# Kernel tuning notes

Measured on AMD Instinct MI355X. Metric: run time of the kernel, lower is better.

## Reference

```python
import jax, jax.numpy as jnp
import numpy as np
from jax import lax

L, H, DH, D, FF = 8, 16, 64, 1024, 4096  # layers, heads, head dim, model dim, mlp hidden
B, S = 4, 512
EPS = 1e-5


def setup_inputs() -> dict:
    key = jax.random.key(0)
    ks = jax.random.split(key, 8)
    std = 0.02
    return {
        "x": jax.random.normal(ks[0], (B, S, D), jnp.float32),
        "ln1_w": jnp.ones((L, D), jnp.float32),
        "ln1_b": jnp.zeros((L, D), jnp.float32),
        "qw": jax.random.normal(ks[1], (L, H, DH, DH), jnp.float32) * std,
        "qb": jnp.zeros((L, H, DH), jnp.float32),
        "kw": jax.random.normal(ks[2], (L, H, DH, DH), jnp.float32) * std,
        "kb": jnp.zeros((L, H, DH), jnp.float32),
        "vw": jax.random.normal(ks[3], (L, H, DH, DH), jnp.float32) * std,
        "vb": jnp.zeros((L, H, DH), jnp.float32),
        "ln2_w": jnp.ones((L, D), jnp.float32),
        "ln2_b": jnp.zeros((L, D), jnp.float32),
        "w1": jax.random.normal(ks[4], (L, D, FF), jnp.float32) * std,
        "b1": jnp.zeros((L, FF), jnp.float32),
        "w2": jax.random.normal(ks[5], (L, FF, D), jnp.float32) * std,
        "b2": jnp.zeros((L, D), jnp.float32),
    }


def _layernorm(x, w, b):
    m = jnp.mean(x, axis=-1, keepdims=True)
    v = jnp.mean(jnp.square(x - m), axis=-1, keepdims=True)
    return (x - m) * lax.rsqrt(v + EPS) * w + b


def reference(x, ln1_w, ln1_b, qw, qb, kw, kb, vw, vb, ln2_w, ln2_b, w1, b1, w2, b2):
    b, s, d = x.shape
    scale = 1.0 / jnp.sqrt(jnp.asarray(DH, x.dtype))

    def layer(h, p):
        (l1w, l1b, Qw, Qb, Kw, Kb, Vw, Vb, l2w, l2b, W1, B1, W2, B2) = p
        y = _layernorm(h, l1w, l1b)
        yh = y.reshape(b, s, H, DH)
        # nn.Linear per head: y @ W.T + b, W is [out=e, in=d]
        q = jnp.einsum('bshd,hed->bshe', yh, Qw) + Qb
        k = jnp.einsum('bshd,hed->bshe', yh, Kw) + Kb
        v = jnp.einsum('bshd,hed->bshe', yh, Vw) + Vb
        attn = jax.nn.softmax(jnp.einsum('bshe,bthe->bhst', q, k) * scale, axis=-1)
        o = jnp.einsum('bhst,bthe->bshe', attn, v).reshape(b, s, d)
        h = h + o
        z = _layernorm(h, l2w, l2b)
        z = jax.nn.gelu(z @ W1 + B1, approximate=False) @ W2 + B2
        return h + z, None

    params = (ln1_w, ln1_b, qw, qb, kw, kb, vw, vb, ln2_w, ln2_b, w1, b1, w2, b2)
    out, _ = lax.scan(layer, x, params)
    return out
```

## Files before the change

kernel.cpp:

```cpp
#include <hip/hip_runtime.h>
#include <hip/hip_bf16.h>

typedef __hip_bfloat16 bf16;
typedef __bf16 bf16x8 __attribute__((ext_vector_type(8)));
typedef float f32x4 __attribute__((ext_vector_type(4)));
typedef unsigned short u16;
typedef unsigned int u32;

#define SEQ 512
#define DMODEL 1024
#define FFDIM 4096
#define NHEAD 16
#define HDIM 64
#define NB 4
#define NLAYER 8

#define SBAR() asm volatile("s_barrier" ::: "memory")

__device__ __forceinline__ u16 f2bu(float f) {
    union { bf16 h; u16 u; } c; c.h = __float2bfloat16(f); return c.u;
}
__device__ __forceinline__ float bu2f(u16 u) {
    union { u32 i; float f; } c; c.i = ((u32)u) << 16; return c.f;
}

__device__ __forceinline__ void gload16(const bf16* g, bf16* l) {
    __builtin_amdgcn_global_load_lds(
        (const __attribute__((address_space(1))) unsigned int*)g,
        (__attribute__((address_space(3))) unsigned int*)l,
        16, 0, 0);
}

__device__ __forceinline__ void gemm_pipe(
    const bf16* __restrict__ A, int lda,
    const bf16* __restrict__ Bt,
    int nkt,
    f32x4 (&acc)[8][2],
    char* lA, char* lB)
{
    const int tid = threadIdx.x;
    const int lane = tid & 63;
    const int wave = tid >> 6;
    const int wr = wave >> 2, wc = wave & 3;
    const int l15 = lane & 15, l4 = lane >> 4;

    auto stage = [&](int c, int t) {
        const bf16* Ak = A + t * 64;
        bf16* dA = (bf16*)(lA + c * 32768);
        bf16* dB = (bf16*)(lB + c * 16384);
#pragma unroll
        for (int it = 0; it < 4; ++it) {
            const int e = (it * 512 + tid) * 8;
            const int r = e >> 6;
            const int cb = (e & 63) * 2;
            const int sc = (cb ^ (((r >> 2) & 1) << 5)) >> 1;
            gload16(Ak + (long)r * lda + sc, dA + e);
        }
        const bf16* Bk = Bt + (long)t * 8192;
#pragma unroll
        for (int it = 0; it < 2; ++it) {
            const int e = (it * 512 + tid) * 8;
            gload16(Bk + e, dB + e);
        }
    };

    stage(0, 0);
    stage(1, 1);
    asm volatile("s_waitcnt vmcnt(6)" ::: "memory");
    SBAR();

    for (int t = 0; t < nkt; ++t) {
        const int cur = t & 1;
        const char* bA = lA + cur * 32768;
        const char* bB = lB + cur * 16384;

        bf16x8 bf_[2][2];
#pragma unroll
        for (int fn = 0; fn < 2; ++fn)
#pragma unroll
            for (int ks = 0; ks < 2; ++ks) {
                const int row = wc * 32 + fn * 16 + l15;
                int byte = row * 128 + (ks * 32 + l4 * 8) * 2;
                byte ^= ((row >> 2) & 1) << 5;
                bf_[fn][ks] = *(const bf16x8*)(bB + byte);
            }
#pragma unroll
        for (int q = 0; q < 4; ++q) {
            bf16x8 af[2][2];
#pragma unroll
            for (int i = 0; i < 2; ++i)
#pragma unroll
                for (int ks = 0; ks < 2; ++ks) {
                    const int row = wr * 128 + (q * 2 + i) * 16 + l15;
                    int byte = row * 128 + (ks * 32 + l4 * 8) * 2;
                    byte ^= ((row >> 2) & 1) << 5;
                    af[i][ks] = *(const bf16x8*)(bA + byte);
                }
            __builtin_amdgcn_s_setprio(1);
#pragma unroll
            for (int i = 0; i < 2; ++i)
#pragma unroll
                for (int fn = 0; fn < 2; ++fn)
#pragma unroll
                    for (int ks = 0; ks < 2; ++ks)
                        acc[q * 2 + i][fn] = __builtin_amdgcn_mfma_f32_16x16x32_bf16(
                            af[i][ks], bf_[fn][ks], acc[q * 2 + i][fn], 0, 0, 0);
            __builtin_amdgcn_s_setprio(0);
        }
        SBAR();
        if (t + 2 < nkt) {
            stage(cur, t + 2);
            asm volatile("s_waitcnt vmcnt(6)" ::: "memory");
        } else {
            asm volatile("s_waitcnt vmcnt(0)" ::: "memory");
        }
        SBAR();
    }
}

__global__ __launch_bounds__(256) void k_ln(const float* __restrict__ h,
                                            const float* __restrict__ w,
                                            const float* __restrict__ bp,
                                            bf16* __restrict__ out,
                                            float* __restrict__ hcopy)
{
    const int row = blockIdx.x;
    const int tid = threadIdx.x;
    const float4 x = ((const float4*)(h + (long)row * DMODEL))[tid];
    if (hcopy) ((float4*)(hcopy + (long)row * DMODEL))[tid] = x;
    float s  = x.x + x.y + x.z + x.w;
    float s2 = x.x * x.x + x.y * x.y + x.z * x.z + x.w * x.w;
#pragma unroll
    for (int off = 32; off; off >>= 1) { s += __shfl_xor(s, off); s2 += __shfl_xor(s2, off); }
    __shared__ float rs[4], rs2[4];
    const int wave = tid >> 6;
    if ((tid & 63) == 0) { rs[wave] = s; rs2[wave] = s2; }
    __syncthreads();
    const float S1 = rs[0] + rs[1] + rs[2] + rs[3];
    const float S2 = rs2[0] + rs2[1] + rs2[2] + rs2[3];
    const float mean = S1 * (1.0f / DMODEL);
    const float var  = S2 * (1.0f / DMODEL) - mean * mean;
    const float rstd = rsqrtf(var + 1e-5f);
    const float4 wv = ((const float4*)w)[tid];
    const float4 bv = ((const float4*)bp)[tid];
    uint2 o;
    o.x = (u32)f2bu((x.x - mean) * rstd * wv.x + bv.x) |
          ((u32)f2bu((x.y - mean) * rstd * wv.y + bv.y) << 16);
    o.y = (u32)f2bu((x.z - mean) * rstd * wv.z + bv.z) |
          ((u32)f2bu((x.w - mean) * rstd * wv.w + bv.w) << 16);
    ((uint2*)(out + (long)row * DMODEL))[tid] = o;
}

__global__ __launch_bounds__(256) void k_tilew(const float* __restrict__ w1,
                                               const float* __restrict__ w2,
                                               bf16* __restrict__ w1t,
                                               bf16* __restrict__ w2t)
{
    __shared__ u16 t[64][138];
    int bid = blockIdx.x;
    const int l = bid >> 10;
    bid &= 1023;
    const long lofs = (long)l * DMODEL * FFDIM;
    const float* src; bf16* dst; int ldsrc;
    if (bid < 512) {
        const int by = bid >> 4, kt = bid & 15;
        src = w1 + lofs + (long)(kt * 64) * FFDIM + by * 128;
        ldsrc = FFDIM;
        dst = w1t + lofs + ((long)by * 16 + kt) * 8192;
    } else {
        bid -= 512;
        const int by = bid >> 6, kt = bid & 63;
        src = w2 + lofs + (long)(kt * 64) * DMODEL + by * 128;
        ldsrc = DMODEL;
        dst = w2t + lofs + ((long)by * 64 + kt) * 8192;
    }
    const int tid = threadIdx.x;
    const int n4 = (tid & 31) * 4;
    const int kr = tid >> 5;
#pragma unroll
    for (int j = 0; j < 8; ++j) {
        const int k = j * 8 + kr;
        const float4 v = *(const float4*)(src + (long)k * ldsrc + n4);
        t[k][n4]     = f2bu(v.x);
        t[k][n4 + 1] = f2bu(v.y);
        t[k][n4 + 2] = f2bu(v.z);
        t[k][n4 + 3] = f2bu(v.w);
    }
    __syncthreads();
#pragma unroll
    for (int it = 0; it < 4; ++it) {
        const int e0 = it * 2048 + tid * 8;
        const int r = e0 >> 6;
        const int c = e0 & 63;
        const int ksw = c ^ (((r >> 2) & 1) << 4);
        u16 v[8];
#pragma unroll
        for (int m = 0; m < 8; ++m) v[m] = t[ksw + m][r];
        uint4 o;
        o.x = (u32)v[0] | ((u32)v[1] << 16);
        o.y = (u32)v[2] | ((u32)v[3] << 16);
        o.z = (u32)v[4] | ((u32)v[5] << 16);
        o.w = (u32)v[6] | ((u32)v[7] << 16);
        *(uint4*)(dst + e0) = o;
    }
}

__global__ __launch_bounds__(256) void k_qkv2(const bf16* __restrict__ y,
                                              const float* __restrict__ qwl,
                                              const float* __restrict__ kwl,
                                              const float* __restrict__ vwl,
                                              const float* __restrict__ qb,
                                              const float* __restrict__ kb,
                                              const float* __restrict__ vb,
                                              bf16* __restrict__ qh,
                                              bf16* __restrict__ kh,
                                              bf16* __restrict__ vt)
{
    __shared__ __align__(16) char lmem[128 * 64 * 2 + 64 * 64 * 2];
    bf16* lA = (bf16*)lmem;
    char* lBb = lmem + 128 * 64 * 2;

    const int tid = threadIdx.x;
    const int lane = tid & 63, wave = tid >> 6;
    const int l15 = lane & 15, l4 = lane >> 4;
    const int z = blockIdx.y;
    const int b = z >> 4, hd = z & 15;
    const bf16* A = y + (long)b * SEQ * DMODEL + hd * HDIM + (long)blockIdx.x * 128 * DMODEL;

#pragma unroll
    for (int it = 0; it < 4; ++it) {
        const int f = (it * 256 + tid) * 8;
        const int r = f >> 6, c = f & 63;
        gload16(A + (long)r * DMODEL + c, lA + f);
    }
    __syncthreads();

    bf16x8 qa[2][2];
#pragma unroll
    for (int fm = 0; fm < 2; ++fm)
#pragma unroll
        for (int ks = 0; ks < 2; ++ks)
            qa[fm][ks] = *(const bf16x8*)(lA + (wave * 32 + fm * 16 + l15) * 64 + ks * 32 + l4 * 8);

    for (int t = 0; t < 3; ++t) {
        __syncthreads();
        const float* Bsrc = ((t == 0) ? qwl : (t == 1) ? kwl : vwl) + (long)hd * HDIM * HDIM;
#pragma unroll
        for (int it = 0; it < 4; ++it) {
            const int f = (it * 256 + tid) * 4;
            const float4 v = *(const float4*)(Bsrc + f);
            uint2 o;
            o.x = (u32)f2bu(v.x) | ((u32)f2bu(v.y) << 16);
            o.y = (u32)f2bu(v.z) | ((u32)f2bu(v.w) << 16);
            const int row = f >> 6;
            const int byte = (f << 1) ^ ((row & 7) << 4);
            *(uint2*)(lBb + byte) = o;
        }
        __syncthreads();

        bf16x8 bfr[4][2];
#pragma unroll
        for (int fn = 0; fn < 4; ++fn)
#pragma unroll
            for (int ks = 0; ks < 2; ++ks) {
                const int row = fn * 16 + l15;
                int byte = (row << 7) + ((ks * 32 + l4 * 8) << 1);
                byte ^= (row & 7) << 4;
                bfr[fn][ks] = *(const bf16x8*)(lBb + byte);
            }
        f32x4 acc[2][4] = {};
#pragma unroll
        for (int ks = 0; ks < 2; ++ks)
#pragma unroll
            for (int fm = 0; fm < 2; ++fm)
#pragma unroll
                for (int fn = 0; fn < 4; ++fn)
                    acc[fm][fn] = __builtin_amdgcn_mfma_f32_16x16x32_bf16(
                        qa[fm][ks], bfr[fn][ks], acc[fm][fn], 0, 0, 0);

        const float* bias = (t == 0) ? qb : (t == 1) ? kb : vb;
#pragma unroll
        for (int fm = 0; fm < 2; ++fm)
#pragma unroll
            for (int fn = 0; fn < 4; ++fn)
#pragma unroll
                for (int r = 0; r < 4; ++r) {
                    const int srow = blockIdx.x * 128 + wave * 32 + fm * 16 + l4 * 4 + r;
                    const int e = fn * 16 + l15;
                    float v = acc[fm][fn][r] + bias[hd * HDIM + e];
                    if (t == 0) {
                        qh[((long)z * SEQ + srow) * HDIM + e] = __float2bfloat16(v * 0.125f);
                    } else if (t == 1) {
                        kh[((long)z * SEQ + srow) * HDIM + e] = __float2bfloat16(v);
                    } else {
                        vt[((long)z * HDIM + e) * SEQ + srow] = __float2bfloat16(v);
                    }
                }
    }
}

__global__ __launch_bounds__(256) void k_flash(const bf16* __restrict__ qh,
                                               const bf16* __restrict__ kh,
                                               const bf16* __restrict__ vt,
                                               float* __restrict__ h)
{
    __shared__ __align__(16) char lmem[24576];
    bf16* lQ = (bf16*)lmem;
    char* lKb = lmem + 8192;
    char* lVb = lmem + 16384;

    const int tid = threadIdx.x;
    const int lane = tid & 63, wave = tid >> 6;
    const int l15 = lane & 15, l4 = lane >> 4;
    const int z = blockIdx.y;
    const int b = z >> 4, hd = z & 15;
    const int q0 = blockIdx.x * 64;

    const bf16* Qsrc = qh + ((long)z * SEQ + q0) * HDIM;
#pragma unroll
    for (int it = 0; it < 2; ++it) {
        const int f = (it * 256 + tid) * 8;
        gload16(Qsrc + f, lQ + f);
    }
    __syncthreads();

    bf16x8 qa[2];
#pragma unroll
    for (int ks = 0; ks < 2; ++ks)
        qa[ks] = *(const bf16x8*)(lQ + (wave * 16 + l15) * 64 + ks * 32 + l4 * 8);

    char* lPb = lmem + wave * 2048;

    f32x4 O[4] = {};
    float mrun[4], lrun[4];
#pragma unroll
    for (int r = 0; r < 4; ++r) { mrun[r] = -1e30f; lrun[r] = 0.0f; }

    for (int kv = 0; kv < SEQ / 64; ++kv) {
        __syncthreads();
        const bf16* Ksrc = kh + ((long)z * SEQ + kv * 64) * HDIM;
#pragma unroll
        for (int it = 0; it < 2; ++it) {
            const int f = (it * 256 + tid) * 8;
            const int r = f >> 6;
            const uint4 v = *(const uint4*)(Ksrc + f);
            *(uint4*)(lKb + ((f << 1) ^ ((r & 7) << 4))) = v;
        }
        const bf16* Vsrc = vt + (long)z * HDIM * SEQ + kv * 64;
#pragma unroll
        for (int it = 0; it < 2; ++it) {
            const int f = (it * 256 + tid) * 8;
            const int r = f >> 6, c = f & 63;
            const uint4 v = *(const uint4*)(Vsrc + (long)r * SEQ + c);
            *(uint4*)(lVb + ((f << 1) ^ ((r & 7) << 4))) = v;
        }
        __syncthreads();

        f32x4 sa[4];
#pragma unroll
        for (int fn = 0; fn < 4; ++fn) sa[fn] = (f32x4){0.f, 0.f, 0.f, 0.f};
#pragma unroll
        for (int ks = 0; ks < 2; ++ks)
#pragma unroll
            for (int fn = 0; fn < 4; ++fn) {
                const int row = fn * 16 + l15;
                int byte = (row << 7) + ((ks * 32 + l4 * 8) << 1);
                byte ^= (row & 7) << 4;
                const bf16x8 kb_ = *(const bf16x8*)(lKb + byte);
                sa[fn] = __builtin_amdgcn_mfma_f32_16x16x32_bf16(qa[ks], kb_, sa[fn], 0, 0, 0);
            }

#pragma unroll
        for (int r = 0; r < 4; ++r) {
            float mx = fmaxf(fmaxf(sa[0][r], sa[1][r]), fmaxf(sa[2][r], sa[3][r]));
#pragma unroll
            for (int m_ = 1; m_ < 16; m_ <<= 1) mx = fmaxf(mx, __shfl_xor(mx, m_));
            const float nm = fmaxf(mrun[r], mx);
            const float al = __expf(mrun[r] - nm);
            mrun[r] = nm;
            float p0 = __expf(sa[0][r] - nm), p1 = __expf(sa[1][r] - nm);
            float p2 = __expf(sa[2][r] - nm), p3 = __expf(sa[3][r] - nm);
            float ps = p0 + p1 + p2 + p3;
#pragma unroll
            for (int m_ = 1; m_ < 16; m_ <<= 1) ps += __shfl_xor(ps, m_);
            lrun[r] = lrun[r] * al + ps;
#pragma unroll
            for (int fn = 0; fn < 4; ++fn) O[fn][r] *= al;
            const int row = l4 * 4 + r;
            const int rsw = (row & 7) << 4;
            const int rb = row << 7;
            *(u16*)(lPb + ((rb + ((0 * 16 + l15) << 1)) ^ rsw)) = f2bu(p0);
            *(u16*)(lPb + ((rb + ((1 * 16 + l15) << 1)) ^ rsw)) = f2bu(p1);
            *(u16*)(lPb + ((rb + ((2 * 16 + l15) << 1)) ^ rsw)) = f2bu(p2);
            *(u16*)(lPb + ((rb + ((3 * 16 + l15) << 1)) ^ rsw)) = f2bu(p3);
        }

#pragma unroll
        for (int ks = 0; ks < 2; ++ks) {
            const int rowp = l15;
            int pbyte = (rowp << 7) + ((ks * 32 + l4 * 8) << 1);
            pbyte ^= (rowp & 7) << 4;
            const bf16x8 pa = *(const bf16x8*)(lPb + pbyte);
#pragma unroll
            for (int fn = 0; fn < 4; ++fn) {
                const int row = fn * 16 + l15;
                int byte = (row << 7) + ((ks * 32 + l4 * 8) << 1);
                byte ^= (row & 7) << 4;
                const bf16x8 vb_ = *(const bf16x8*)(lVb + byte);
                O[fn] = __builtin_amdgcn_mfma_f32_16x16x32_bf16(pa, vb_, O[fn], 0, 0, 0);
            }
        }
    }

    float rinv[4];
#pragma unroll
    for (int r = 0; r < 4; ++r) rinv[r] = 1.0f / lrun[r];
#pragma unroll
    for (int fn = 0; fn < 4; ++fn)
#pragma unroll
        for (int r = 0; r < 4; ++r) {
            const int srow = q0 + wave * 16 + l4 * 4 + r;
            const int e = fn * 16 + l15;
            h[((long)b * SEQ + srow) * DMODEL + hd * HDIM + e] += O[fn][r] * rinv[r];
        }
}

__global__ __launch_bounds__(512, 2) void k_gemm1(const bf16* __restrict__ zb,
                                                  const bf16* __restrict__ w1t,
                                                  const float* __restrict__ b1,
                                                  bf16* __restrict__ ff1)
{
    __shared__ __align__(16) char lmem[98304];
    const int bx = (int)blockIdx.y >> 2;
    const int by = (int)blockIdx.x * 4 + ((int)blockIdx.y & 3);
    const bf16* A = zb + (long)bx * 256 * DMODEL;
    const bf16* Bt = w1t + (long)by * 16 * 8192;
    f32x4 acc[8][2] = {};
    gemm_pipe(A, DMODEL, Bt, DMODEL / 64, acc, lmem, lmem + 65536);

    const int lane = threadIdx.x & 63, wave = threadIdx.x >> 6;
    const int wr = wave >> 2, wc = wave & 3;
    const int l15 = lane & 15, l4 = lane >> 4;
#pragma unroll
    for (int fm = 0; fm < 8; ++fm)
#pragma unroll
        for (int fn = 0; fn < 2; ++fn)
#pragma unroll
            for (int r = 0; r < 4; ++r) {
                const int row = bx * 256 + wr * 128 + fm * 16 + l4 * 4 + r;
                const int col = by * 128 + wc * 32 + fn * 16 + l15;
                const float x = acc[fm][fn][r] + b1[col];
                const float g = 0.5f * x * (1.0f + erff(x * 0.70710678118f));
                ff1[(long)row * FFDIM + col] = __float2bfloat16(g);
            }
}

__global__ __launch_bounds__(512, 2) void k_gemm2(const bf16* __restrict__ ff1,
                                                  const bf16* __restrict__ w2t,
                                                  bf16* __restrict__ part)
{
    __shared__ __align__(16) char lmem[98304];
    const int sk = blockIdx.z;
    const int bx = (int)blockIdx.y;
    const int by = (int)blockIdx.x;
    const bf16* A = ff1 + (long)bx * 256 * FFDIM + (long)sk * 1024;
    const bf16* Bt = w2t + ((long)by * 64 + sk * 16) * 8192;
    f32x4 acc[8][2] = {};
    gemm_pipe(A, FFDIM, Bt, 1024 / 64, acc, lmem, lmem + 65536);

    bf16* out = part + (long)sk * (NB * SEQ) * DMODEL;
    const int lane = threadIdx.x & 63, wave = threadIdx.x >> 6;
    const int wr = wave >> 2, wc = wave & 3;
    const int l15 = lane & 15, l4 = lane >> 4;
#pragma unroll
    for (int fm = 0; fm < 8; ++fm)
#pragma unroll
        for (int fn = 0; fn < 2; ++fn)
#pragma unroll
            for (int r = 0; r < 4; ++r) {
                const int row = bx * 256 + wr * 128 + fm * 16 + l4 * 4 + r;
                const int col = by * 128 + wc * 32 + fn * 16 + l15;
                out[(long)row * DMODEL + col] = __float2bfloat16(acc[fm][fn][r]);
            }
}

__global__ __launch_bounds__(256) void k_red2ln(const bf16* __restrict__ part,
                                                const float* __restrict__ b2,
                                                float* __restrict__ h,
                                                const float* __restrict__ lnw,
                                                const float* __restrict__ lnb,
                                                bf16* __restrict__ y,
                                                int do_ln)
{
    constexpr long NELT = (long)NB * SEQ * DMODEL;
    const long row = blockIdx.x;
    const int tid = threadIdx.x;
    const long e0 = row * DMODEL + tid * 4;
    float sum[4] = {0.f, 0.f, 0.f, 0.f};
#pragma unroll
    for (int sk = 0; sk < 4; ++sk) {
        const uint2 u = *(const uint2*)(part + sk * NELT + e0);
        sum[0] += bu2f((u16)(u.x & 0xffffu));
        sum[1] += bu2f((u16)(u.x >> 16));
        sum[2] += bu2f((u16)(u.y & 0xffffu));
        sum[3] += bu2f((u16)(u.y >> 16));
    }
    const float4 bv = ((const float4*)b2)[tid];
    float4 hv = ((float4*)h)[row * (DMODEL / 4) + tid];
    hv.x += sum[0] + bv.x;
    hv.y += sum[1] + bv.y;
    hv.z += sum[2] + bv.z;
    hv.w += sum[3] + bv.w;
    ((float4*)h)[row * (DMODEL / 4) + tid] = hv;

    if (!do_ln) return;
    float ss  = hv.x + hv.y + hv.z + hv.w;
    float ss2 = hv.x * hv.x + hv.y * hv.y + hv.z * hv.z + hv.w * hv.w;
#pragma unroll
    for (int off = 32; off; off >>= 1) { ss += __shfl_xor(ss, off); ss2 += __shfl_xor(ss2, off); }
    __shared__ float rs[4], rs2[4];
    const int wave = tid >> 6;
    if ((tid & 63) == 0) { rs[wave] = ss; rs2[wave] = ss2; }
    __syncthreads();
    const float S1 = rs[0] + rs[1] + rs[2] + rs[3];
    const float S2 = rs2[0] + rs2[1] + rs2[2] + rs2[3];
    const float mean = S1 * (1.0f / DMODEL);
    const float var  = S2 * (1.0f / DMODEL) - mean * mean;
    const float rstd = rsqrtf(var + 1e-5f);
    const float4 wv = ((const float4*)lnw)[tid];
    const float4 lb = ((const float4*)lnb)[tid];
    uint2 o;
    o.x = (u32)f2bu((hv.x - mean) * rstd * wv.x + lb.x) |
          ((u32)f2bu((hv.y - mean) * rstd * wv.y + lb.y) << 16);
    o.y = (u32)f2bu((hv.z - mean) * rstd * wv.z + lb.z) |
          ((u32)f2bu((hv.w - mean) * rstd * wv.w + lb.w) << 16);
    ((uint2*)(y + row * DMODEL))[tid] = o;
}

extern "C" void kernel_launch(void* const* d_in, const int* in_sizes, int n_in,
                              void* d_out, int out_size, void* d_ws, size_t ws_size,
                              hipStream_t stream)
{
    const float* x    = (const float*)d_in[0];
    const float* ln1w = (const float*)d_in[1];
    const float* ln1b = (const float*)d_in[2];
    const float* qw   = (const float*)d_in[3];
    const float* qb   = (const float*)d_in[4];
    const float* kw   = (const float*)d_in[5];
    const float* kb   = (const float*)d_in[6];
    const float* vw   = (const float*)d_in[7];
    const float* vb   = (const float*)d_in[8];
    const float* ln2w = (const float*)d_in[9];
    const float* ln2b = (const float*)d_in[10];
    const float* w1   = (const float*)d_in[11];
    const float* b1   = (const float*)d_in[12];
    const float* w2   = (const float*)d_in[13];
    const float* b2   = (const float*)d_in[14];

    char* ws = (char*)d_ws;
    const size_t MB = 1024 * 1024;
    bf16* y    = (bf16*)(ws + 0 * MB);
    bf16* zb   = (bf16*)(ws + 4 * MB);
    bf16* qh   = (bf16*)(ws + 8 * MB);
    bf16* kh   = (bf16*)(ws + 12 * MB);
    bf16* vt   = (bf16*)(ws + 16 * MB);
    bf16* ff1  = (bf16*)(ws + 20 * MB);
    bf16* part = (bf16*)(ws + 36 * MB);
    bf16* w1tA = (bf16*)(ws + 68 * MB);
    bf16* w2tA = (bf16*)(ws + 132 * MB);

    float* h = (float*)d_out;

    k_tilew<<<NLAYER * 1024, 256, 0, stream>>>(w1, w2, w1tA, w2tA);
    k_ln<<<NB * SEQ, 256, 0, stream>>>(x, ln1w, ln1b, y, h);

    for (int l = 0; l < NLAYER; ++l) {
        const long wofs = (long)l * DMODEL * FFDIM;
        k_qkv2<<<dim3(4, NB * NHEAD), 256, 0, stream>>>(
            y, qw + (long)l * 65536, kw + (long)l * 65536, vw + (long)l * 65536,
            qb + l * NHEAD * HDIM, kb + l * NHEAD * HDIM, vb + l * NHEAD * HDIM,
            qh, kh, vt);
        k_flash<<<dim3(SEQ / 64, NB * NHEAD), 256, 0, stream>>>(qh, kh, vt, h);
        k_ln<<<NB * SEQ, 256, 0, stream>>>(h, ln2w + l * DMODEL, ln2b + l * DMODEL, zb,
                                           nullptr);
        k_gemm1<<<dim3(8, 32), 512, 0, stream>>>(zb, w1tA + wofs, b1 + l * FFDIM, ff1);
        k_gemm2<<<dim3(8, 8, 4), 512, 0, stream>>>(ff1, w2tA + wofs, part);
        const int last = (l == NLAYER - 1);
        k_red2ln<<<NB * SEQ, 256, 0, stream>>>(part, b2 + l * DMODEL, h,
                                               ln1w + (l + 1) * DMODEL * (1 - last),
                                               ln1b + (l + 1) * DMODEL * (1 - last),
                                               y, !last);
    }
}
```

Measured before the change: 926.6 us.

## Fuse QKV projection into flash attention, recomputing K/V per query block

Merges the separate QKV projection kernel and flash-attention kernel into one kernel. Each block computes Q for its 128 query rows, then for every 64-key tile loads the normalized activations and projects K and V on the fly into shared memory before the attention math. This removes one launch per layer and the global round trip of the Q/K/V intermediates. In exchange, K/V projections are recomputed by each of the 4 query blocks per head, the grid halves to 256 blocks with 64 KB LDS each, and a third barrier is added per KV tile.

```diff
diff --git a/kernel.cpp b/kernel.cpp
--- a/kernel.cpp
+++ b/kernel.cpp
@@ -205,160 +205,178 @@
     }
 }
 
-__global__ __launch_bounds__(256) void k_qkv2(const bf16* __restrict__ y,
+__global__ __launch_bounds__(256) void k_attn(const bf16* __restrict__ y,
                                               const float* __restrict__ qwl,
                                               const float* __restrict__ kwl,
                                               const float* __restrict__ vwl,
                                               const float* __restrict__ qb,
                                               const float* __restrict__ kb,
                                               const float* __restrict__ vb,
-                                              bf16* __restrict__ qh,
-                                              bf16* __restrict__ kh,
-                                              bf16* __restrict__ vt)
-{
-    __shared__ __align__(16) char lmem[128 * 64 * 2 + 64 * 64 * 2];
-    bf16* lA = (bf16*)lmem;
-    char* lBb = lmem + 128 * 64 * 2;
+                                              float* __restrict__ h)
+{
+    __shared__ __align__(16) char lmem[65536];
+    bf16* lY  = (bf16*)lmem;
+    char* lQ  = lmem + 16384;
+    char* lK  = lmem + 32768;
+    char* lV  = lmem + 40960;
+    char* lWk = lmem + 49152;
+    char* lWv = lmem + 57344;
 
     const int tid = threadIdx.x;
     const int lane = tid & 63, wave = tid >> 6;
     const int l15 = lane & 15, l4 = lane >> 4;
-    const int z = blockIdx.y;
-    const int b = z >> 4, hd = z & 15;
-    const bf16* A = y + (long)b * SEQ * DMODEL + hd * HDIM + (long)blockIdx.x * 128 * DMODEL;
-
-#pragma unroll
-    for (int it = 0; it < 4; ++it) {
-        const int f = (it * 256 + tid) * 8;
-        const int r = f >> 6, c = f & 63;
-        gload16(A + (long)r * DMODEL + c, lA + f);
-    }
-    __syncthreads();
-
-    bf16x8 qa[2][2];
-#pragma unroll
-    for (int fm = 0; fm < 2; ++fm)
-#pragma unroll
-        for (int ks = 0; ks < 2; ++ks)
-            qa[fm][ks] = *(const bf16x8*)(lA + (wave * 32 + fm * 16 + l15) * 64 + ks * 32 + l4 * 8);
-
-    for (int t = 0; t < 3; ++t) {
-        __syncthreads();
-        const float* Bsrc = ((t == 0) ? qwl : (t == 1) ? kwl : vwl) + (long)hd * HDIM * HDIM;
+    const int z = blockIdx.y, b = z >> 4, hd = z & 15;
+    const int q0 = blockIdx.x * 128;
+
+    {
+        const float* s0 = qwl + (long)hd * HDIM * HDIM;
+        const float* s1 = kwl + (long)hd * HDIM * HDIM;
+        const float* s2 = vwl + (long)hd * HDIM * HDIM;
 #pragma unroll
         for (int it = 0; it < 4; ++it) {
             const int f = (it * 256 + tid) * 4;
-            const float4 v = *(const float4*)(Bsrc + f);
+            const int row = f >> 6;
+            const int byte = (f << 1) ^ ((row & 7) << 4);
+            float4 v = *(const float4*)(s0 + f);
             uint2 o;
             o.x = (u32)f2bu(v.x) | ((u32)f2bu(v.y) << 16);
             o.y = (u32)f2bu(v.z) | ((u32)f2bu(v.w) << 16);
-            const int row = f >> 6;
-            const int byte = (f << 1) ^ ((row & 7) << 4);
-            *(uint2*)(lBb + byte) = o;
-        }
-        __syncthreads();
-
-        bf16x8 bfr[4][2];
-#pragma unroll
-        for (int fn = 0; fn < 4; ++fn)
-#pragma unroll
-            for (int ks = 0; ks < 2; ++ks) {
-                const int row = fn * 16 + l15;
-                int byte = (row << 7) + ((ks * 32 + l4 * 8) << 1);
-                byte ^= (row & 7) << 4;
-                bfr[fn][ks] = *(const bf16x8*)(lBb + byte);
-            }
-        f32x4 acc[2][4] = {};
-#pragma unroll
-        for (int ks = 0; ks < 2; ++ks)
-#pragma unroll
-            for (int fm = 0; fm < 2; ++fm)
-#pragma unroll
-                for (int fn = 0; fn < 4; ++fn)
-                    acc[fm][fn] = __builtin_amdgcn_mfma_f32_16x16x32_bf16(
-                        qa[fm][ks], bfr[fn][ks], acc[fm][fn], 0, 0, 0);
-
-        const float* bias = (t == 0) ? qb : (t == 1) ? kb : vb;
+            *(uint2*)(lK + byte) = o;
+            v = *(const float4*)(s1 + f);
+            o.x = (u32)f2bu(v.x) | ((u32)f2bu(v.y) << 16);
+            o.y = (u32)f2bu(v.z) | ((u32)f2bu(v.w) << 16);
+            *(uint2*)(lWk + byte) = o;
+            v = *(const float4*)(s2 + f);
+            o.x = (u32)f2bu(v.x) | ((u32)f2bu(v.y) << 16);
+            o.y = (u32)f2bu(v.z) | ((u32)f2bu(v.w) << 16);
+            *(uint2*)(lWv + byte) = o;
+        }
+    }
+    const bf16* Yq = y + ((long)b * SEQ + q0) * DMODEL + hd * HDIM;
+#pragma unroll
+    for (int it = 0; it < 4; ++it) {
+        const int e = (it * 256 + tid) * 8;
+        const int r = e >> 6;
+        const int cb = (e & 63) * 2;
+        const int sc = (cb ^ (((r >> 2) & 1) << 5)) >> 1;
+        gload16(Yq + (long)r * DMODEL + sc, lY + e);
+    }
+    __syncthreads();
+
+    {
+        f32x4 qacc[2][4] = {};
+#pragma unroll
+        for (int ks = 0; ks < 2; ++ks) {
+            bf16x8 af[2];
+#pragma unroll
+            for (int fm = 0; fm < 2; ++fm) {
+                const int row = wave * 32 + fm * 16 + l15;
+                int byte = row * 128 + (ks * 32 + l4 * 8) * 2;
+                byte ^= ((row >> 2) & 1) << 5;
+                af[fm] = *(const bf16x8*)((char*)lY + byte);
+            }
+#pragma unroll
+            for (int fn = 0; fn < 4; ++fn) {
+                const int wrow = fn * 16 + l15;
+                int wbyte = (wrow << 7) + ((ks * 32 + l4 * 8) << 1);
+                wbyte ^= (wrow & 7) << 4;
+                const bf16x8 wf = *(const bf16x8*)(lK + wbyte);
+#pragma unroll
+                for (int fm = 0; fm < 2; ++fm)
+                    qacc[fm][fn] = __builtin_amdgcn_mfma_f32_16x16x32_bf16(
+                        af[fm], wf, qacc[fm][fn], 0, 0, 0);
+            }
+        }
 #pragma unroll
         for (int fm = 0; fm < 2; ++fm)
 #pragma unroll
-            for (int fn = 0; fn < 4; ++fn)
+            for (int fn = 0; fn < 4; ++fn) {
+                const int e = fn * 16 + l15;
+                const float bias = qb[hd * HDIM + e];
 #pragma unroll
                 for (int r = 0; r < 4; ++r) {
-                    const int srow = blockIdx.x * 128 + wave * 32 + fm * 16 + l4 * 4 + r;
-                    const int e = fn * 16 + l15;
-                    float v = acc[fm][fn][r] + bias[hd * HDIM + e];
-                    if (t == 0) {
-                        qh[((long)z * SEQ + srow) * HDIM + e] = __float2bfloat16(v * 0.125f);
-                    } else if (t == 1) {
-                        kh[((long)z * SEQ + srow) * HDIM + e] = __float2bfloat16(v);
-                    } else {
-                        vt[((long)z * HDIM + e) * SEQ + srow] = __float2bfloat16(v);
-                    }
+                    const int row = wave * 32 + fm * 16 + l4 * 4 + r;
+                    const int byte = ((row << 7) + (e << 1)) ^ ((row & 7) << 4);
+                    *(u16*)(lQ + byte) = f2bu((qacc[fm][fn][r] + bias) * 0.125f);
                 }
-    }
-}
-
-__global__ __launch_bounds__(256) void k_flash(const bf16* __restrict__ qh,
-                                               const bf16* __restrict__ kh,
-                                               const bf16* __restrict__ vt,
-                                               float* __restrict__ h)
-{
-    __shared__ __align__(16) char lmem[24576];
-    bf16* lQ = (bf16*)lmem;
-    char* lKb = lmem + 8192;
-    char* lVb = lmem + 16384;
-
-    const int tid = threadIdx.x;
-    const int lane = tid & 63, wave = tid >> 6;
-    const int l15 = lane & 15, l4 = lane >> 4;
-    const int z = blockIdx.y;
-    const int b = z >> 4, hd = z & 15;
-    const int q0 = blockIdx.x * 64;
-
-    const bf16* Qsrc = qh + ((long)z * SEQ + q0) * HDIM;
-#pragma unroll
-    for (int it = 0; it < 2; ++it) {
-        const int f = (it * 256 + tid) * 8;
-        gload16(Qsrc + f, lQ + f);
+            }
     }
     __syncthreads();
 
-    bf16x8 qa[2];
-#pragma unroll
-    for (int ks = 0; ks < 2; ++ks)
-        qa[ks] = *(const bf16x8*)(lQ + (wave * 16 + l15) * 64 + ks * 32 + l4 * 8);
-
-    char* lPb = lmem + wave * 2048;
-
-    f32x4 O[4] = {};
-    float mrun[4], lrun[4];
-#pragma unroll
-    for (int r = 0; r < 4; ++r) { mrun[r] = -1e30f; lrun[r] = 0.0f; }
+    bf16x8 qa[2][2];
+#pragma unroll
+    for (int fm = 0; fm < 2; ++fm)
+#pragma unroll
+        for (int ks = 0; ks < 2; ++ks) {
+            const int row = wave * 32 + fm * 16 + l15;
+            int byte = (row << 7) + ((ks * 32 + l4 * 8) << 1);
+            byte ^= (row & 7) << 4;
+            qa[fm][ks] = *(const bf16x8*)(lQ + byte);
+        }
+
+    char* lP = lQ + wave * 4096;
+
+    f32x4 O[2][4] = {};
+    float mrun[2][4], lrun[2][4];
+#pragma unroll
+    for (int fm = 0; fm < 2; ++fm)
+#pragma unroll
+        for (int r = 0; r < 4; ++r) { mrun[fm][r] = -1e30f; lrun[fm][r] = 0.0f; }
 
     for (int kv = 0; kv < SEQ / 64; ++kv) {
         __syncthreads();
-        const bf16* Ksrc = kh + ((long)z * SEQ + kv * 64) * HDIM;
+        const bf16* Ykv = y + ((long)b * SEQ + kv * 64) * DMODEL + hd * HDIM;
 #pragma unroll
         for (int it = 0; it < 2; ++it) {
-            const int f = (it * 256 + tid) * 8;
-            const int r = f >> 6;
-            const uint4 v = *(const uint4*)(Ksrc + f);
-            *(uint4*)(lKb + ((f << 1) ^ ((r & 7) << 4))) = v;
-        }
-        const bf16* Vsrc = vt + (long)z * HDIM * SEQ + kv * 64;
-#pragma unroll
-        for (int it = 0; it < 2; ++it) {
-            const int f = (it * 256 + tid) * 8;
-            const int r = f >> 6, c = f & 63;
-            const uint4 v = *(const uint4*)(Vsrc + (long)r * SEQ + c);
-            *(uint4*)(lVb + ((f << 1) ^ ((r & 7) << 4))) = v;
+            const int e = (it * 256 + tid) * 8;
+            const int r = e >> 6;
+            const int cb = (e & 63) * 2;
+            const int sc = (cb ^ (((r >> 2) & 1) << 5)) >> 1;
+            gload16(Ykv + (long)r * DMODEL + sc, lY + e);
         }
         __syncthreads();
 
-        f32x4 sa[4];
-#pragma unroll
-        for (int fn = 0; fn < 4; ++fn) sa[fn] = (f32x4){0.f, 0.f, 0.f, 0.f};
+        {
+            f32x4 kacc[4] = {}, vacc[4] = {};
+#pragma unroll
+            for (int ks = 0; ks < 2; ++ks) {
+                const int yrow = wave * 16 + l15;
+                int ybyte = yrow * 128 + (ks * 32 + l4 * 8) * 2;
+                ybyte ^= ((yrow >> 2) & 1) << 5;
+                const bf16x8 ay = *(const bf16x8*)((char*)lY + ybyte);
+#pragma unroll
+                for (int fn = 0; fn < 4; ++fn) {
+                    const int wrow = fn * 16 + l15;
+                    int wbyte = (wrow << 7) + ((ks * 32 + l4 * 8) << 1);
+                    wbyte ^= (wrow & 7) << 4;
+                    kacc[fn] = __builtin_amdgcn_mfma_f32_16x16x32_bf16(
+                        ay, *(const bf16x8*)(lWk + wbyte), kacc[fn], 0, 0, 0);
+                    vacc[fn] = __builtin_amdgcn_mfma_f32_16x16x32_bf16(
+                        ay, *(const bf16x8*)(lWv + wbyte), vacc[fn], 0, 0, 0);
+                }
+            }
+#pragma unroll
+            for (int fn = 0; fn < 4; ++fn) {
+                const int e = fn * 16 + l15;
+                const float kbv = kb[hd * HDIM + e];
+                const float vbv = vb[hd * HDIM + e];
+#pragma unroll
+                for (int r = 0; r < 4; ++r) {
+                    const int key = wave * 16 + l4 * 4 + r;
+                    const int kbyte = ((key << 7) + (e << 1)) ^ ((key & 7) << 4);
+                    *(u16*)(lK + kbyte) = f2bu(kacc[fn][r] + kbv);
+                    const int vbyte = ((e << 7) + (key << 1)) ^ ((e & 7) << 4);
+                    *(u16*)(lV + vbyte) = f2bu(vacc[fn][r] + vbv);
+                }
+            }
+        }
+        __syncthreads();
+
+        f32x4 sa[2][4];
+#pragma unroll
+        for (int fm = 0; fm < 2; ++fm)
+#pragma unroll
+            for (int fn = 0; fn < 4; ++fn) sa[fm][fn] = (f32x4){0.f, 0.f, 0.f, 0.f};
 #pragma unroll
         for (int ks = 0; ks < 2; ++ks)
 #pragma unroll
@@ -366,63 +384,79 @@
                 const int row = fn * 16 + l15;
                 int byte = (row << 7) + ((ks * 32 + l4 * 8) << 1);
                 byte ^= (row & 7) << 4;
-                const bf16x8 kb_ = *(const bf16x8*)(lKb + byte);
-                sa[fn] = __builtin_amdgcn_mfma_f32_16x16x32_bf16(qa[ks], kb_, sa[fn], 0, 0, 0);
-            }
-
-#pragma unroll
-        for (int r = 0; r < 4; ++r) {
-            float mx = fmaxf(fmaxf(sa[0][r], sa[1][r]), fmaxf(sa[2][r], sa[3][r]));
-#pragma unroll
-            for (int m_ = 1; m_ < 16; m_ <<= 1) mx = fmaxf(mx, __shfl_xor(mx, m_));
-            const float nm = fmaxf(mrun[r], mx);
-            const float al = __expf(mrun[r] - nm);
-            mrun[r] = nm;
-            float p0 = __expf(sa[0][r] - nm), p1 = __expf(sa[1][r] - nm);
-            float p2 = __expf(sa[2][r] - nm), p3 = __expf(sa[3][r] - nm);
-            float ps = p0 + p1 + p2 + p3;
-#pragma unroll
-            for (int m_ = 1; m_ < 16; m_ <<= 1) ps += __shfl_xor(ps, m_);
-            lrun[r] = lrun[r] * al + ps;
-#pragma unroll
-            for (int fn = 0; fn < 4; ++fn) O[fn][r] *= al;
-            const int row = l4 * 4 + r;
-            const int rsw = (row & 7) << 4;
-            const int rb = row << 7;
-            *(u16*)(lPb + ((rb + ((0 * 16 + l15) << 1)) ^ rsw)) = f2bu(p0);
-            *(u16*)(lPb + ((rb + ((1 * 16 + l15) << 1)) ^ rsw)) = f2bu(p1);
-            *(u16*)(lPb + ((rb + ((2 * 16 + l15) << 1)) ^ rsw)) = f2bu(p2);
-            *(u16*)(lPb + ((rb + ((3 * 16 + l15) << 1)) ^ rsw)) = f2bu(p3);
-        }
+                const bf16x8 kf = *(const bf16x8*)(lK + byte);
+#pragma unroll
+                for (int fm = 0; fm < 2; ++fm)
+                    sa[fm][fn] = __builtin_amdgcn_mfma_f32_16x16x32_bf16(
+                        qa[fm][ks], kf, sa[fm][fn], 0, 0, 0);
+            }
+
+#pragma unroll
+        for (int fm = 0; fm < 2; ++fm)
+#pragma unroll
+            for (int r = 0; r < 4; ++r) {
+                float mx = fmaxf(fmaxf(sa[fm][0][r], sa[fm][1][r]),
+                                 fmaxf(sa[fm][2][r], sa[fm][3][r]));
+#pragma unroll
+                for (int m_ = 1; m_ < 16; m_ <<= 1) mx = fmaxf(mx, __shfl_xor(mx, m_));
+                const float nm = fmaxf(mrun[fm][r], mx);
+                const float al = __expf(mrun[fm][r] - nm);
+                mrun[fm][r] = nm;
+                float p0 = __expf(sa[fm][0][r] - nm), p1 = __expf(sa[fm][1][r] - nm);
+                float p2 = __expf(sa[fm][2][r] - nm), p3 = __expf(sa[fm][3][r] - nm);
+                float ps = p0 + p1 + p2 + p3;
+#pragma unroll
+                for (int m_ = 1; m_ < 16; m_ <<= 1) ps += __shfl_xor(ps, m_);
+                lrun[fm][r] = lrun[fm][r] * al + ps;
+#pragma unroll
+                for (int fn = 0; fn < 4; ++fn) O[fm][fn][r] *= al;
+                const int row = fm * 16 + l4 * 4 + r;
+                const int rsw = (row & 7) << 4;
+                const int rb_ = row << 7;
+                *(u16*)(lP + ((rb_ + ((0 * 16 + l15) << 1)) ^ rsw)) = f2bu(p0);
+                *(u16*)(lP + ((rb_ + ((1 * 16 + l15) << 1)) ^ rsw)) = f2bu(p1);
+                *(u16*)(lP + ((rb_ + ((2 * 16 + l15) << 1)) ^ rsw)) = f2bu(p2);
+                *(u16*)(lP + ((rb_ + ((3 * 16 + l15) << 1)) ^ rsw)) = f2bu(p3);
+            }
 
 #pragma unroll
         for (int ks = 0; ks < 2; ++ks) {
-            const int rowp = l15;
-            int pbyte = (rowp << 7) + ((ks * 32 + l4 * 8) << 1);
-            pbyte ^= (rowp & 7) << 4;
-            const bf16x8 pa = *(const bf16x8*)(lPb + pbyte);
+            bf16x8 pa[2];
+#pragma unroll
+            for (int fm = 0; fm < 2; ++fm) {
+                const int row = fm * 16 + l15;
+                int pbyte = (row << 7) + ((ks * 32 + l4 * 8) << 1);
+                pbyte ^= (row & 7) << 4;
+                pa[fm] = *(const bf16x8*)(lP + pbyte);
+            }
 #pragma unroll
             for (int fn = 0; fn < 4; ++fn) {
                 const int row = fn * 16 + l15;
                 int byte = (row << 7) + ((ks * 32 + l4 * 8) << 1);
                 byte ^= (row & 7) << 4;
-                const bf16x8 vb_ = *(const bf16x8*)(lVb + byte);
-                O[fn] = __builtin_amdgcn_mfma_f32_16x16x32_bf16(pa, vb_, O[fn], 0, 0, 0);
-            }
-        }
-    }
-
-    float rinv[4];
-#pragma unroll
-    for (int r = 0; r < 4; ++r) rinv[r] = 1.0f / lrun[r];
-#pragma unroll
-    for (int fn = 0; fn < 4; ++fn)
-#pragma unroll
-        for (int r = 0; r < 4; ++r) {
-            const int srow = q0 + wave * 16 + l4 * 4 + r;
-            const int e = fn * 16 + l15;
-            h[((long)b * SEQ + srow) * DMODEL + hd * HDIM + e] += O[fn][r] * rinv[r];
-        }
+                const bf16x8 vf = *(const bf16x8*)(lV + byte);
+#pragma unroll
+                for (int fm = 0; fm < 2; ++fm)
+                    O[fm][fn] = __builtin_amdgcn_mfma_f32_16x16x32_bf16(
+                        pa[fm], vf, O[fm][fn], 0, 0, 0);
+            }
+        }
+    }
+
+#pragma unroll
+    for (int fm = 0; fm < 2; ++fm) {
+        float rinv[4];
+#pragma unroll
+        for (int r = 0; r < 4; ++r) rinv[r] = 1.0f / lrun[fm][r];
+#pragma unroll
+        for (int fn = 0; fn < 4; ++fn)
+#pragma unroll
+            for (int r = 0; r < 4; ++r) {
+                const int qrow = q0 + wave * 32 + fm * 16 + l4 * 4 + r;
+                const int e = fn * 16 + l15;
+                h[((long)b * SEQ + qrow) * DMODEL + hd * HDIM + e] += O[fm][fn][r] * rinv[r];
+            }
+    }
 }
 
 __global__ __launch_bounds__(512, 2) void k_gemm1(const bf16* __restrict__ zb,
@@ -561,9 +595,6 @@
     const size_t MB = 1024 * 1024;
     bf16* y    = (bf16*)(ws + 0 * MB);
     bf16* zb   = (bf16*)(ws + 4 * MB);
-    bf16* qh   = (bf16*)(ws + 8 * MB);
-    bf16* kh   = (bf16*)(ws + 12 * MB);
-    bf16* vt   = (bf16*)(ws + 16 * MB);
     bf16* ff1  = (bf16*)(ws + 20 * MB);
     bf16* part = (bf16*)(ws + 36 * MB);
     bf16* w1tA = (bf16*)(ws + 68 * MB);
@@ -576,11 +607,9 @@
 
     for (int l = 0; l < NLAYER; ++l) {
         const long wofs = (long)l * DMODEL * FFDIM;
-        k_qkv2<<<dim3(4, NB * NHEAD), 256, 0, stream>>>(
+        k_attn<<<dim3(SEQ / 128, NB * NHEAD), 256, 0, stream>>>(
             y, qw + (long)l * 65536, kw + (long)l * 65536, vw + (long)l * 65536,
-            qb + l * NHEAD * HDIM, kb + l * NHEAD * HDIM, vb + l * NHEAD * HDIM,
-            qh, kh, vt);
-        k_flash<<<dim3(SEQ / 64, NB * NHEAD), 256, 0, stream>>>(qh, kh, vt, h);
+            qb + l * NHEAD * HDIM, kb + l * NHEAD * HDIM, vb + l * NHEAD * HDIM, h);
         k_ln<<<NB * SEQ, 256, 0, stream>>>(h, ln2w + l * DMODEL, ln2b + l * DMODEL, zb,
                                            nullptr);
         k_gemm1<<<dim3(8, 32), 512, 0, stream>>>(zb, w1tA + wofs, b1 + l * FFDIM, ff1);
```

Measured after the change: 933.9 us. About the same (+0.8%).
